# Performance work log

Hardware: AMD Instinct MI355X
Metric: run time of the kernel (lower is better)

Reference implementation:

```python
import jax, jax.numpy as jnp
import numpy as np

DIM = 1024
HEADS = 16
HEAD_DIM = DIM // HEADS  # 64


def get_rope_matrix(seq_len: int, dim: int) -> jnp.ndarray:
    # rope[s, d] = concat(cos(s * inv_freq), sin(s * inv_freq))  -> (seq_len, dim)
    half = dim // 2
    inv_freq = 1.0 / (10000.0 ** (jnp.arange(half, dtype=jnp.float32) / half))
    sinusoid = jnp.arange(seq_len, dtype=jnp.float32)[:, None] * inv_freq[None, :]
    return jnp.concatenate([jnp.cos(sinusoid), jnp.sin(sinusoid)], axis=-1)


def setup_inputs() -> dict:
    key = jax.random.key(0)
    ks = jax.random.split(key, 6)
    B, T, D = 2, 2048, DIM
    scale = 1.0 / np.sqrt(D)
    return {
        "x": jax.random.normal(ks[0], (B, T, D), dtype=jnp.float32),
        "Wq": jax.random.normal(ks[1], (D, D), dtype=jnp.float32) * scale,
        "Wk": jax.random.normal(ks[2], (D, D), dtype=jnp.float32) * scale,
        "Wv": jax.random.normal(ks[3], (D, D), dtype=jnp.float32) * scale,
        "Wo": jax.random.normal(ks[4], (D, D), dtype=jnp.float32) * scale,
        "bo": jax.random.normal(ks[5], (D,), dtype=jnp.float32) * 0.01,
    }


def reference(x, Wq, Wk, Wv, Wo, bo):
    B, T, D = x.shape
    H, hd = HEADS, HEAD_DIM

    # projections -> (B, H, T, hd)
    def split_heads(y):
        return y.reshape(B, T, H, hd).transpose(0, 2, 1, 3)

    q = split_heads(x @ Wq)
    k = split_heads(x @ Wk)
    v = split_heads(x @ Wv)

    rope = get_rope_matrix(T, hd)  # (T, hd)

    # apply_rope(v, rope): einsum('...nd,sd->...ns') contracts head_dim -> (B,H,T,T)
    v_r = jnp.einsum('bhnd,sd->bhns', v, rope)

    scores = jax.nn.softmax(jnp.einsum('bhnd,bhmd->bhnm', q, k) / jnp.sqrt(jnp.float32(hd)), axis=-1)
    out = jnp.einsum('bhnm,bhms->bhns', scores, v_r)  # (B,H,T,T)

    # apply_rope(out, rope.T): out2[...,n,s] = sum_t out[...,n,t] * rope[t,s] -> (B,H,T,hd)
    out = jnp.einsum('bhnt,ts->bhns', out, rope)

    out = out.transpose(0, 2, 1, 3).reshape(B, T, D)
    return out @ Wo + bo
```

## Files before the change

kernel.cpp:

```cpp
#include <hip/hip_runtime.h>
#include <math.h>

#define DIM 1024
#define NH 16
#define HD 64
#define TT 2048
#define NTOK 4096

typedef __bf16 bf8v __attribute__((ext_vector_type(8)));
typedef float f4v __attribute__((ext_vector_type(4)));
typedef float f16v __attribute__((ext_vector_type(16)));
typedef unsigned short us8 __attribute__((ext_vector_type(8)));
typedef unsigned short us4 __attribute__((ext_vector_type(4)));
typedef unsigned int u4v __attribute__((ext_vector_type(4)));

static __device__ __forceinline__ unsigned short f2bf(float f) {
    unsigned int u = __float_as_uint(f);
    u += 0x7FFFu + ((u >> 16) & 1u);
    return (unsigned short)(u >> 16);
}
static __device__ __forceinline__ bf8v ld8(const unsigned short* p) {
    return __builtin_bit_cast(bf8v, *(const us8*)p);
}
static __device__ __forceinline__ void gl_lds(const unsigned short* g, unsigned short* l) {
    __builtin_amdgcn_global_load_lds((const __attribute__((address_space(1))) unsigned int*)(g),
                                     (__attribute__((address_space(3))) unsigned int*)(l), 16, 0, 0);
}

__global__ void k_prep(const float* __restrict__ x, unsigned short* __restrict__ xb,
                       const float* __restrict__ Wq, const float* __restrict__ Wk,
                       const float* __restrict__ Wv, unsigned short* __restrict__ wt,
                       float* __restrict__ rope) {
    int tid = threadIdx.x;
    int bb = blockIdx.x;
    if (bb < 4096) {
        int i = bb * 256 + tid;
        float4 v = ((const float4*)x)[i];
        us4 o;
        o[0] = f2bf(v.x); o[1] = f2bf(v.y); o[2] = f2bf(v.z); o[3] = f2bf(v.w);
        *(us4*)&xb[i * 4] = o;
    } else if (bb < 7168) {
        __shared__ float tile[32][33];
        bb -= 4096;
        int z = bb >> 10, rem = bb & 1023;
        int bx = rem & 31, by = rem >> 5;
        const float* W = (z == 0) ? Wq : ((z == 1) ? Wk : Wv);
        int tx = tid & 31, ty = tid >> 5;
        int c0 = bx * 32, k0 = by * 32;
#pragma unroll
        for (int j = 0; j < 4; j++)
            tile[ty + j * 8][tx] = W[(k0 + ty + j * 8) * DIM + c0 + tx];
        __syncthreads();
        unsigned short* out = wt + z * DIM * DIM;
#pragma unroll
        for (int j = 0; j < 4; j++)
            out[(c0 + ty + j * 8) * DIM + k0 + tx] = f2bf(tile[tx][ty + j * 8]);
    } else {
        int i = (bb - 7168) * 256 + tid;
        int s = i >> 6, d = i & 63;
        float inv = exp2f(-(float)(d & 31) * (13.287712379549449f / 32.0f));
        float a = (float)s * inv;
        rope[i] = (d < 32) ? cosf(a) : sinf(a);
    }
}

__global__ void k_R(const float* __restrict__ rope, float* __restrict__ R) {
    __shared__ float red[256];
    int d = blockIdx.x;
    int e = threadIdx.x & 63, sl = threadIdx.x >> 6;
    const float* rp = rope + sl * 512 * 64;
    float acc = 0.f;
    for (int s = 0; s < 512; s++)
        acc += rp[s * 64 + d] * rp[s * 64 + e];
    red[threadIdx.x] = acc;
    __syncthreads();
    if (sl == 0)
        R[d * 64 + e] = (red[e] + red[e + 64]) + (red[e + 128] + red[e + 192]);
}

__global__ void k_wo2(const float* __restrict__ Wo, const float* __restrict__ R,
                      unsigned short* __restrict__ wo2t) {
    __shared__ float Ws[64 * 65];
    __shared__ float Rt[64 * 65];
    int tid = threadIdx.x;
    int h = blockIdx.y, j0 = blockIdx.x * 64;
    for (int idx = tid; idx < 4096; idx += 256) {
        int e = idx >> 6, j = idx & 63;
        Ws[e * 65 + j] = Wo[(h * 64 + e) * DIM + j0 + j];
        Rt[e * 65 + j] = R[j * 64 + e];
    }
    __syncthreads();
    int d = tid & 63, jb = (tid >> 6) * 16;
    float acc[16] = {};
    for (int e = 0; e < 64; e++) {
        float r = Rt[e * 65 + d];
#pragma unroll
        for (int jj = 0; jj < 16; jj++)
            acc[jj] += r * Ws[e * 65 + jb + jj];
    }
#pragma unroll
    for (int jj = 0; jj < 16; jj++)
        wo2t[(j0 + jb + jj) * DIM + h * 64 + d] = f2bf(acc[jj]);
}


__global__ __launch_bounds__(256, 3) void k_gemm_qkv(const unsigned short* __restrict__ A,
                                                     const unsigned short* __restrict__ Bt,
                                                     unsigned short* __restrict__ qk,
                                                     unsigned short* __restrict__ vt) {
    __shared__ unsigned short As[128 * 32];
    __shared__ unsigned short Bs[128 * 32];
    const int K = 1024;
    int tid = threadIdx.x;
    int lane = tid & 63, w = tid >> 6;
    int quad = lane >> 4, l16 = lane & 15;
    int m0 = blockIdx.y * 128, n0 = blockIdx.x * 128;
    int wm = (w >> 1) * 64, wn = (w & 1) * 64;

    int s0 = tid, s1 = 256 + tid;
    int r0 = s0 >> 2, cc0 = ((s0 & 3) ^ (r0 & 3)) * 8;
    int r1 = s1 >> 2, cc1 = ((s1 & 3) ^ (r1 & 3)) * 8;
    const unsigned short* Ag0 = A + (m0 + r0) * K + cc0;
    const unsigned short* Ag1 = A + (m0 + r1) * K + cc1;
    const unsigned short* Bg0 = Bt + (n0 + r0) * K + cc0;
    const unsigned short* Bg1 = Bt + (n0 + r1) * K + cc1;
    int qx = quad ^ (l16 & 3);

    f4v acc[4][4] = {};
    for (int k0 = 0; k0 < K; k0 += 32) {
        __syncthreads();
        gl_lds(Ag0 + k0, &As[s0 * 8]);
        gl_lds(Ag1 + k0, &As[s1 * 8]);
        gl_lds(Bg0 + k0, &Bs[s0 * 8]);
        gl_lds(Bg1 + k0, &Bs[s1 * 8]);
        __syncthreads();
        bf8v af[4], bf[4];
#pragma unroll
        for (int mt = 0; mt < 4; mt++)
            af[mt] = ld8(&As[(wm + mt * 16 + l16) * 32 + qx * 8]);
#pragma unroll
        for (int nt = 0; nt < 4; nt++)
            bf[nt] = ld8(&Bs[(wn + nt * 16 + l16) * 32 + qx * 8]);
#pragma unroll
        for (int mt = 0; mt < 4; mt++)
#pragma unroll
            for (int nt = 0; nt < 4; nt++)
                acc[mt][nt] = __builtin_amdgcn_mfma_f32_16x16x32_bf16(af[mt], bf[nt], acc[mt][nt], 0, 0, 0);
    }
#pragma unroll
    for (int mt = 0; mt < 4; mt++) {
#pragma unroll
        for (int nt = 0; nt < 4; nt++) {
            int gc = n0 + wn + nt * 16 + l16;
            int h = (gc >> 6) & 15;
            int d = gc & 63;
            if (gc < 2048) {
                float qs = (gc < 1024) ? 0.18033688011111793f : 1.0f;
                int mtx = gc >> 10;
                unsigned short* base = qk + mtx * (NTOK * DIM);
#pragma unroll
                for (int r = 0; r < 4; r++) {
                    int gm = m0 + wm + mt * 16 + quad * 4 + r;
                    int b = gm >> 11, t = gm & 2047;
                    base[((b * NH + h) * TT + t) * HD + d] = f2bf(acc[mt][nt][r] * qs);
                }
            } else {
                int gm0 = m0 + wm + mt * 16 + quad * 4;
                int b = gm0 >> 11, t = gm0 & 2047;
                us4 ov;
#pragma unroll
                for (int r = 0; r < 4; r++)
                    ov[r] = f2bf(acc[mt][nt][r]);
                *(us4*)&vt[(((b * NH + h) * HD) + d) * TT + t] = ov;
            }
        }
    }
}

__global__ __launch_bounds__(256, 3) void k_gemm_out(const unsigned short* __restrict__ A,
                                                     const unsigned short* __restrict__ Bt,
                                                     const float* __restrict__ bo,
                                                     float* __restrict__ out) {
    __shared__ unsigned short As[128 * 32];
    __shared__ unsigned short Bs[128 * 32];
    const int K = 1024;
    int tid = threadIdx.x;
    int lane = tid & 63, w = tid >> 6;
    int quad = lane >> 4, l16 = lane & 15;
    int m0 = blockIdx.y * 128, n0 = blockIdx.x * 128;
    int wm = (w >> 1) * 64, wn = (w & 1) * 64;

    int s0 = tid, s1 = 256 + tid;
    int r0 = s0 >> 2, cc0 = ((s0 & 3) ^ (r0 & 3)) * 8;
    int r1 = s1 >> 2, cc1 = ((s1 & 3) ^ (r1 & 3)) * 8;
    const unsigned short* Ag0 = A + (m0 + r0) * K + cc0;
    const unsigned short* Ag1 = A + (m0 + r1) * K + cc1;
    const unsigned short* Bg0 = Bt + (n0 + r0) * K + cc0;
    const unsigned short* Bg1 = Bt + (n0 + r1) * K + cc1;
    int qx = quad ^ (l16 & 3);

    f4v acc[4][4] = {};
    for (int k0 = 0; k0 < K; k0 += 32) {
        __syncthreads();
        gl_lds(Ag0 + k0, &As[s0 * 8]);
        gl_lds(Ag1 + k0, &As[s1 * 8]);
        gl_lds(Bg0 + k0, &Bs[s0 * 8]);
        gl_lds(Bg1 + k0, &Bs[s1 * 8]);
        __syncthreads();
        bf8v af[4], bf[4];
#pragma unroll
        for (int mt = 0; mt < 4; mt++)
            af[mt] = ld8(&As[(wm + mt * 16 + l16) * 32 + qx * 8]);
#pragma unroll
        for (int nt = 0; nt < 4; nt++)
            bf[nt] = ld8(&Bs[(wn + nt * 16 + l16) * 32 + qx * 8]);
#pragma unroll
        for (int mt = 0; mt < 4; mt++)
#pragma unroll
            for (int nt = 0; nt < 4; nt++)
                acc[mt][nt] = __builtin_amdgcn_mfma_f32_16x16x32_bf16(af[mt], bf[nt], acc[mt][nt], 0, 0, 0);
    }
#pragma unroll
    for (int mt = 0; mt < 4; mt++) {
#pragma unroll
        for (int nt = 0; nt < 4; nt++) {
            int gc = n0 + wn + nt * 16 + l16;
            float bias = bo[gc];
#pragma unroll
            for (int r = 0; r < 4; r++) {
                int gm = m0 + wm + mt * 16 + quad * 4 + r;
                out[gm * DIM + gc] = acc[mt][nt][r] + bias;
            }
        }
    }
}

__global__ __launch_bounds__(256, 2) void k_flash(const unsigned short* __restrict__ qk,
                                                  const unsigned short* __restrict__ vt,
                                                  unsigned short* __restrict__ Op,
                                                  float* __restrict__ Ls) {
    __shared__ unsigned short Ks[2][64 * 64];
    __shared__ unsigned short Vs[2][64 * 64];
    int tid = threadIdx.x;
    int lane = tid & 63, w = tid >> 6;
    int q31 = lane & 31, hi = lane >> 5;
    int bid = blockIdx.x;
    int xcd = bid & 7, sl = bid >> 3;
    int bh = xcd * 4 + (sl & 3);
    int qt = (sl >> 2) & 7;
    int sp = sl >> 5;

    const unsigned short* Qg = qk + bh * (TT * HD);
    const unsigned short* Kg = qk + NTOK * DIM + bh * (TT * HD) + sp * 1024 * HD;
    const unsigned short* Vg = vt + bh * (HD * TT) + sp * 1024;

    int qr0 = qt * 256 + w * 64 + q31;
    bf8v qf[2][4];
#pragma unroll
    for (int g = 0; g < 2; g++)
#pragma unroll
        for (int ks = 0; ks < 4; ks++)
            qf[g][ks] = ld8(Qg + (qr0 + g * 32) * HD + ks * 16 + hi * 8);

    int r0 = tid >> 3, sw = (tid & 7) ^ (r0 & 7);
    int offK0 = r0 * HD + sw * 8, offK1 = offK0 + 32 * HD;
    int offV0 = r0 * TT + sw * 8, offV1 = offV0 + 32 * TT;
    int dst0 = tid * 8, dst1 = dst0 + 2048;

#define STAGE(tile, bufsel) do {                                  \
        const unsigned short* kb_ = Kg + (tile) * 64 * HD;        \
        const unsigned short* vb_ = Vg + (tile) * 64;             \
        gl_lds(kb_ + offK0, &Ks[bufsel][dst0]);                   \
        gl_lds(kb_ + offK1, &Ks[bufsel][dst1]);                   \
        gl_lds(vb_ + offV0, &Vs[bufsel][dst0]);                   \
        gl_lds(vb_ + offV1, &Vs[bufsel][dst1]);                   \
    } while (0)

    STAGE(0, 0);
    STAGE(1, 1);

    f16v oacc[2][2] = {};
    float lsg[2] = {0.f, 0.f};
    int xsw = q31 & 7;

    for (int it = 0; it < 16; it++) {
        int cur = it & 1;
        if (it == 15) { asm volatile("s_waitcnt vmcnt(0)" ::: "memory"); }
        else          { asm volatile("s_waitcnt vmcnt(4)" ::: "memory"); }
        __builtin_amdgcn_s_barrier();
        asm volatile("" ::: "memory");

        const unsigned short* Kb = Ks[cur];
        const unsigned short* Vb = Vs[cur];
        bf8v pb[2][4];

#pragma unroll
        for (int mt = 0; mt < 2; mt++) {
            bf8v kf[4];
#pragma unroll
            for (int ks = 0; ks < 4; ks++)
                kf[ks] = ld8(&Kb[(mt * 32 + q31) * 64 + ((2 * ks + hi) ^ xsw) * 8]);
            f16v sg0 = {}, sg1 = {};
            __builtin_amdgcn_s_setprio(1);
#pragma unroll
            for (int ks = 0; ks < 4; ks++) {
                sg0 = __builtin_amdgcn_mfma_f32_32x32x16_bf16(kf[ks], qf[0][ks], sg0, 0, 0, 0);
                sg1 = __builtin_amdgcn_mfma_f32_32x32x16_bf16(kf[ks], qf[1][ks], sg1, 0, 0, 0);
            }
            __builtin_amdgcn_s_setprio(0);
#pragma unroll
            for (int g = 0; g < 2; g++) {
                f16v s = g ? sg1 : sg0;
#pragma unroll
                for (int sub = 0; sub < 2; sub++) {
                    float pe[8];
#pragma unroll
                    for (int j = 0; j < 8; j++) {
                        pe[j] = __builtin_amdgcn_exp2f(s[sub * 8 + j]);
                        lsg[g] += pe[j];
                    }
                    unsigned int e0, e1, e2, e3;
                    asm("v_cvt_pk_bf16_f32 %0, %1, %2" : "=v"(e0) : "v"(pe[0]), "v"(pe[1]));
                    asm("v_cvt_pk_bf16_f32 %0, %1, %2" : "=v"(e1) : "v"(pe[2]), "v"(pe[3]));
                    asm("v_cvt_pk_bf16_f32 %0, %1, %2" : "=v"(e2) : "v"(pe[4]), "v"(pe[5]));
                    asm("v_cvt_pk_bf16_f32 %0, %1, %2" : "=v"(e3) : "v"(pe[6]), "v"(pe[7]));
                    asm("v_permlane32_swap_b32 %0, %1" : "+v"(e0), "+v"(e2));
                    asm("v_permlane32_swap_b32 %0, %1" : "+v"(e1), "+v"(e3));
                    u4v pv = {e0, e1, e2, e3};
                    pb[g][mt * 2 + sub] = __builtin_bit_cast(bf8v, pv);
                }
            }
        }

#pragma unroll
        for (int mtd = 0; mtd < 2; mtd++) {
            bf8v vf[4];
#pragma unroll
            for (int kk = 0; kk < 4; kk++)
                vf[kk] = ld8(&Vb[(mtd * 32 + q31) * 64 + ((2 * kk + hi) ^ xsw) * 8]);
            __builtin_amdgcn_s_setprio(1);
#pragma unroll
            for (int kk = 0; kk < 4; kk++) {
                oacc[0][mtd] = __builtin_amdgcn_mfma_f32_32x32x16_bf16(vf[kk], pb[0][kk], oacc[0][mtd], 0, 0, 0);
                oacc[1][mtd] = __builtin_amdgcn_mfma_f32_32x32x16_bf16(vf[kk], pb[1][kk], oacc[1][mtd], 0, 0, 0);
            }
            __builtin_amdgcn_s_setprio(0);
        }

        __builtin_amdgcn_s_barrier();
        asm volatile("" ::: "memory");
        if (it < 14) STAGE(it + 2, cur);
    }
#undef STAGE

    int b = bh >> 4, h = bh & 15;
#pragma unroll
    for (int g = 0; g < 2; g++) {
        float lsum = lsg[g] + __shfl_xor(lsg[g], 32, 64);
        int qrow = qr0 + g * 32;
        unsigned short* dst = Op + sp * (NTOK * DIM) + ((b * TT) + qrow) * DIM + h * HD + hi * 4;
#pragma unroll
        for (int mtd = 0; mtd < 2; mtd++) {
#pragma unroll
            for (int g4 = 0; g4 < 4; g4++) {
                us4 ov;
#pragma unroll
                for (int r = 0; r < 4; r++)
                    ov[r] = f2bf(oacc[g][mtd][g4 * 4 + r]);
                *(us4*)&dst[mtd * 32 + g4 * 8] = ov;
            }
        }
        if (hi == 0)
            Ls[sp * 65536 + bh * 2048 + qrow] = lsum;
    }
}

__global__ void k_comb(const unsigned short* __restrict__ Op, const float* __restrict__ Ls,
                       unsigned short* __restrict__ attn) {
    int e = (blockIdx.x * 256 + threadIdx.x) * 8;
    int h = (e >> 6) & 15, t = (e >> 10) & 2047, b = e >> 21;
    int bh = b * 16 + h;
    float inv = 1.0f / (Ls[bh * 2048 + t] + Ls[65536 + bh * 2048 + t]);
    us8 a = *(const us8*)&Op[e];
    us8 c = *(const us8*)&Op[NTOK * DIM + e];
    us8 o;
#pragma unroll
    for (int j = 0; j < 8; j++) {
        float fa = __uint_as_float((unsigned int)a[j] << 16);
        float fc = __uint_as_float((unsigned int)c[j] << 16);
        o[j] = f2bf((fa + fc) * inv);
    }
    *(us8*)&attn[e] = o;
}

extern "C" void kernel_launch(void* const* d_in, const int* in_sizes, int n_in,
                              void* d_out, int out_size, void* d_ws, size_t ws_size,
                              hipStream_t stream) {
    const float* x  = (const float*)d_in[0];
    const float* Wq = (const float*)d_in[1];
    const float* Wk = (const float*)d_in[2];
    const float* Wv = (const float*)d_in[3];
    const float* Wo = (const float*)d_in[4];
    const float* bo = (const float*)d_in[5];
    float* out = (float*)d_out;
    char* ws = (char*)d_ws;

    unsigned short* Xb    = (unsigned short*)(ws);
    unsigned short* Wqkvt = (unsigned short*)(ws + 8388608);
    unsigned short* Op    = (unsigned short*)(ws);
    unsigned short* QK    = (unsigned short*)(ws + 16777216);
    unsigned short* Vt    = (unsigned short*)(ws + 33554432);
    unsigned short* attn  = (unsigned short*)(ws + 41943040);
    unsigned short* Wo2t  = (unsigned short*)(ws + 50331648);
    float*          rope  = (float*)(ws + 52428800);
    float*          Rm    = (float*)(ws + 52953088);
    float*          Ls    = (float*)(ws + 52969472);

    hipLaunchKernelGGL(k_prep,     dim3(7680),   dim3(256), 0, stream, x, Xb, Wq, Wk, Wv, Wqkvt, rope);
    hipLaunchKernelGGL(k_R,        dim3(64),     dim3(256), 0, stream, rope, Rm);
    hipLaunchKernelGGL(k_wo2,      dim3(16, 16), dim3(256), 0, stream, Wo, Rm, Wo2t);
    hipLaunchKernelGGL(k_gemm_qkv, dim3(24, 32), dim3(256), 0, stream, Xb, Wqkvt, QK, Vt);
    hipLaunchKernelGGL(k_flash,    dim3(512),    dim3(256), 0, stream, QK, Vt, Op, Ls);
    hipLaunchKernelGGL(k_comb,     dim3(2048),   dim3(256), 0, stream, Op, Ls, attn);
    hipLaunchKernelGGL(k_gemm_out, dim3(8, 32),  dim3(256), 0, stream, attn, Wo2t, bo, out);
}
```

Baseline: 219.7 us.

## Halve flash query tile per wave to double grid and occupancy

Each wave in the flash kernel now handles 32 query rows instead of 64, so the grid doubles to 1024 blocks and launch bounds are raised to 4 blocks per SM. The P·V MFMAs are now issued right after each exp/convert step instead of after all of P is built, and the setprio hints are removed. This cuts register pressure and raises occupancy, but each K/V tile staged in LDS is reused by half as many query rows, which roughly doubles K/V load traffic.

```diff
diff --git a/kernel.cpp b/kernel.cpp
--- a/kernel.cpp
+++ b/kernel.cpp
@@ -235,7 +235,7 @@
     }
 }
 
-__global__ __launch_bounds__(256, 2) void k_flash(const unsigned short* __restrict__ qk,
+__global__ __launch_bounds__(256, 4) void k_flash(const unsigned short* __restrict__ qk,
                                                   const unsigned short* __restrict__ vt,
                                                   unsigned short* __restrict__ Op,
                                                   float* __restrict__ Ls) {
@@ -247,20 +247,18 @@
     int bid = blockIdx.x;
     int xcd = bid & 7, sl = bid >> 3;
     int bh = xcd * 4 + (sl & 3);
-    int qt = (sl >> 2) & 7;
-    int sp = sl >> 5;
+    int qt = (sl >> 2) & 15;
+    int sp = sl >> 6;
 
     const unsigned short* Qg = qk + bh * (TT * HD);
     const unsigned short* Kg = qk + NTOK * DIM + bh * (TT * HD) + sp * 1024 * HD;
     const unsigned short* Vg = vt + bh * (HD * TT) + sp * 1024;
 
-    int qr0 = qt * 256 + w * 64 + q31;
-    bf8v qf[2][4];
-#pragma unroll
-    for (int g = 0; g < 2; g++)
-#pragma unroll
-        for (int ks = 0; ks < 4; ks++)
-            qf[g][ks] = ld8(Qg + (qr0 + g * 32) * HD + ks * 16 + hi * 8);
+    int qrow = qt * 128 + w * 32 + q31;
+    bf8v qf[4];
+#pragma unroll
+    for (int ks = 0; ks < 4; ks++)
+        qf[ks] = ld8(Qg + qrow * HD + ks * 16 + hi * 8);
 
     int r0 = tid >> 3, sw = (tid & 7) ^ (r0 & 7);
     int offK0 = r0 * HD + sw * 8, offK1 = offK0 + 32 * HD;
@@ -279,8 +277,8 @@
     STAGE(0, 0);
     STAGE(1, 1);
 
-    f16v oacc[2][2] = {};
-    float lsg[2] = {0.f, 0.f};
+    f16v oacc[2] = {};
+    float lsg = 0.f;
     int xsw = q31 & 7;
 
     for (int it = 0; it < 16; it++) {
@@ -292,59 +290,52 @@
 
         const unsigned short* Kb = Ks[cur];
         const unsigned short* Vb = Vs[cur];
-        bf8v pb[2][4];
+
+        bf8v kf0[4], kf1[4];
+#pragma unroll
+        for (int ks = 0; ks < 4; ks++) {
+            kf0[ks] = ld8(&Kb[(q31) * 64 + ((2 * ks + hi) ^ xsw) * 8]);
+            kf1[ks] = ld8(&Kb[(32 + q31) * 64 + ((2 * ks + hi) ^ xsw) * 8]);
+        }
+        f16v s0 = {}, s1 = {};
+#pragma unroll
+        for (int ks = 0; ks < 4; ks++) {
+            s0 = __builtin_amdgcn_mfma_f32_32x32x16_bf16(kf0[ks], qf[ks], s0, 0, 0, 0);
+            s1 = __builtin_amdgcn_mfma_f32_32x32x16_bf16(kf1[ks], qf[ks], s1, 0, 0, 0);
+        }
+
+        bf8v vf[2][4];
+#pragma unroll
+        for (int kk = 0; kk < 4; kk++) {
+            vf[0][kk] = ld8(&Vb[(q31) * 64 + ((2 * kk + hi) ^ xsw) * 8]);
+            vf[1][kk] = ld8(&Vb[(32 + q31) * 64 + ((2 * kk + hi) ^ xsw) * 8]);
+        }
 
 #pragma unroll
         for (int mt = 0; mt < 2; mt++) {
-            bf8v kf[4];
-#pragma unroll
-            for (int ks = 0; ks < 4; ks++)
-                kf[ks] = ld8(&Kb[(mt * 32 + q31) * 64 + ((2 * ks + hi) ^ xsw) * 8]);
-            f16v sg0 = {}, sg1 = {};
-            __builtin_amdgcn_s_setprio(1);
-#pragma unroll
-            for (int ks = 0; ks < 4; ks++) {
-                sg0 = __builtin_amdgcn_mfma_f32_32x32x16_bf16(kf[ks], qf[0][ks], sg0, 0, 0, 0);
-                sg1 = __builtin_amdgcn_mfma_f32_32x32x16_bf16(kf[ks], qf[1][ks], sg1, 0, 0, 0);
+#pragma unroll
+            for (int sub = 0; sub < 2; sub++) {
+                const f16v& s = mt ? s1 : s0;
+                float pe[8];
+#pragma unroll
+                for (int j = 0; j < 8; j++)
+                    pe[j] = __builtin_amdgcn_exp2f(s[sub * 8 + j]);
+                float t01 = pe[0] + pe[1], t23 = pe[2] + pe[3];
+                float t45 = pe[4] + pe[5], t67 = pe[6] + pe[7];
+                lsg += (t01 + t23) + (t45 + t67);
+                unsigned int e0, e1, e2, e3;
+                asm("v_cvt_pk_bf16_f32 %0, %1, %2" : "=v"(e0) : "v"(pe[0]), "v"(pe[1]));
+                asm("v_cvt_pk_bf16_f32 %0, %1, %2" : "=v"(e1) : "v"(pe[2]), "v"(pe[3]));
+                asm("v_cvt_pk_bf16_f32 %0, %1, %2" : "=v"(e2) : "v"(pe[4]), "v"(pe[5]));
+                asm("v_cvt_pk_bf16_f32 %0, %1, %2" : "=v"(e3) : "v"(pe[6]), "v"(pe[7]));
+                asm("v_permlane32_swap_b32 %0, %1" : "+v"(e0), "+v"(e2));
+                asm("v_permlane32_swap_b32 %0, %1" : "+v"(e1), "+v"(e3));
+                u4v pv = {e0, e1, e2, e3};
+                bf8v pb = __builtin_bit_cast(bf8v, pv);
+                int kk = mt * 2 + sub;
+                oacc[0] = __builtin_amdgcn_mfma_f32_32x32x16_bf16(vf[0][kk], pb, oacc[0], 0, 0, 0);
+                oacc[1] = __builtin_amdgcn_mfma_f32_32x32x16_bf16(vf[1][kk], pb, oacc[1], 0, 0, 0);
             }
-            __builtin_amdgcn_s_setprio(0);
-#pragma unroll
-            for (int g = 0; g < 2; g++) {
-                f16v s = g ? sg1 : sg0;
-#pragma unroll
-                for (int sub = 0; sub < 2; sub++) {
-                    float pe[8];
-#pragma unroll
-                    for (int j = 0; j < 8; j++) {
-                        pe[j] = __builtin_amdgcn_exp2f(s[sub * 8 + j]);
-                        lsg[g] += pe[j];
-                    }
-                    unsigned int e0, e1, e2, e3;
-                    asm("v_cvt_pk_bf16_f32 %0, %1, %2" : "=v"(e0) : "v"(pe[0]), "v"(pe[1]));
-                    asm("v_cvt_pk_bf16_f32 %0, %1, %2" : "=v"(e1) : "v"(pe[2]), "v"(pe[3]));
-                    asm("v_cvt_pk_bf16_f32 %0, %1, %2" : "=v"(e2) : "v"(pe[4]), "v"(pe[5]));
-                    asm("v_cvt_pk_bf16_f32 %0, %1, %2" : "=v"(e3) : "v"(pe[6]), "v"(pe[7]));
-                    asm("v_permlane32_swap_b32 %0, %1" : "+v"(e0), "+v"(e2));
-                    asm("v_permlane32_swap_b32 %0, %1" : "+v"(e1), "+v"(e3));
-                    u4v pv = {e0, e1, e2, e3};
-                    pb[g][mt * 2 + sub] = __builtin_bit_cast(bf8v, pv);
-                }
-            }
-        }
-
-#pragma unroll
-        for (int mtd = 0; mtd < 2; mtd++) {
-            bf8v vf[4];
-#pragma unroll
-            for (int kk = 0; kk < 4; kk++)
-                vf[kk] = ld8(&Vb[(mtd * 32 + q31) * 64 + ((2 * kk + hi) ^ xsw) * 8]);
-            __builtin_amdgcn_s_setprio(1);
-#pragma unroll
-            for (int kk = 0; kk < 4; kk++) {
-                oacc[0][mtd] = __builtin_amdgcn_mfma_f32_32x32x16_bf16(vf[kk], pb[0][kk], oacc[0][mtd], 0, 0, 0);
-                oacc[1][mtd] = __builtin_amdgcn_mfma_f32_32x32x16_bf16(vf[kk], pb[1][kk], oacc[1][mtd], 0, 0, 0);
-            }
-            __builtin_amdgcn_s_setprio(0);
         }
 
         __builtin_amdgcn_s_barrier();
@@ -353,26 +344,22 @@
     }
 #undef STAGE
 
+    float lsum = lsg + __shfl_xor(lsg, 32, 64);
     int b = bh >> 4, h = bh & 15;
-#pragma unroll
-    for (int g = 0; g < 2; g++) {
-        float lsum = lsg[g] + __shfl_xor(lsg[g], 32, 64);
-        int qrow = qr0 + g * 32;
-        unsigned short* dst = Op + sp * (NTOK * DIM) + ((b * TT) + qrow) * DIM + h * HD + hi * 4;
-#pragma unroll
-        for (int mtd = 0; mtd < 2; mtd++) {
-#pragma unroll
-            for (int g4 = 0; g4 < 4; g4++) {
-                us4 ov;
-#pragma unroll
-                for (int r = 0; r < 4; r++)
-                    ov[r] = f2bf(oacc[g][mtd][g4 * 4 + r]);
-                *(us4*)&dst[mtd * 32 + g4 * 8] = ov;
-            }
-        }
-        if (hi == 0)
-            Ls[sp * 65536 + bh * 2048 + qrow] = lsum;
-    }
+    unsigned short* dst = Op + sp * (NTOK * DIM) + ((b * TT) + qrow) * DIM + h * HD + hi * 4;
+#pragma unroll
+    for (int mtd = 0; mtd < 2; mtd++) {
+#pragma unroll
+        for (int g4 = 0; g4 < 4; g4++) {
+            us4 ov;
+#pragma unroll
+            for (int r = 0; r < 4; r++)
+                ov[r] = f2bf(oacc[mtd][g4 * 4 + r]);
+            *(us4*)&dst[mtd * 32 + g4 * 8] = ov;
+        }
+    }
+    if (hi == 0)
+        Ls[sp * 65536 + bh * 2048 + qrow] = lsum;
 }
 
 __global__ void k_comb(const unsigned short* __restrict__ Op, const float* __restrict__ Ls,
@@ -420,7 +407,7 @@
     hipLaunchKernelGGL(k_R,        dim3(64),     dim3(256), 0, stream, rope, Rm);
     hipLaunchKernelGGL(k_wo2,      dim3(16, 16), dim3(256), 0, stream, Wo, Rm, Wo2t);
     hipLaunchKernelGGL(k_gemm_qkv, dim3(24, 32), dim3(256), 0, stream, Xb, Wqkvt, QK, Vt);
-    hipLaunchKernelGGL(k_flash,    dim3(512),    dim3(256), 0, stream, QK, Vt, Op, Ls);
+    hipLaunchKernelGGL(k_flash,    dim3(1024),   dim3(256), 0, stream, QK, Vt, Op, Ls);
     hipLaunchKernelGGL(k_comb,     dim3(2048),   dim3(256), 0, stream, Op, Ls, attn);
     hipLaunchKernelGGL(k_gemm_out, dim3(8, 32),  dim3(256), 0, stream, attn, Wo2t, bo, out);
 }
```

Result: no change. 221.2 us (+0.7%).
